# Kernel tuning notes

Measured on AMD Instinct MI355X. Metric: run time of the kernel, lower is better.

The kernel has to match this reference:

```python
import jax, jax.numpy as jnp
import numpy as np

C = 256  # channels
SHAPES = [(8, C, 80, 80), (8, C, 40, 40), (8, C, 20, 20), (8, C, 10, 10)]
EPS = 1e-8  # torch cosine_similarity eps


def _nearest_resize(x, H, W):
    # Matches F.interpolate(mode='nearest'): src_idx = floor(dst_idx * in/out)
    b, c, h, w = x.shape
    rows = (jnp.arange(H) * h) // H
    cols = (jnp.arange(W) * w) // W
    return x[:, :, rows[:, None], cols[None, :]]


def setup_inputs() -> dict:
    key = jax.random.key(0)
    ks = jax.random.split(key, 12)
    d = {}
    for i, s in enumerate(SHAPES):
        d[f"f{i}"] = jax.random.normal(ks[i], s, dtype=jnp.float32)
        d[f"w{i}"] = jax.random.normal(ks[4 + i], (C, C), dtype=jnp.float32) / jnp.sqrt(jnp.float32(C))
        d[f"b{i}"] = jax.random.normal(ks[8 + i], (C,), dtype=jnp.float32) * 0.01
    return d


def reference(f0, f1, f2, f3, w0, w1, w2, w3, b0, b1, b2, b3):
    feats = [f0, f1, f2, f3]
    ws = [w0, w1, w2, w3]
    bs = [b0, b1, b2, b3]
    H = max(f.shape[2] for f in feats)
    W = max(f.shape[3] for f in feats)
    proj = []
    for f, w, b in zip(feats, ws, bs):
        # 1x1 conv == per-pixel GEMM over channels
        p = jnp.einsum('bchw,oc->bohw', f, w) + b[None, :, None, None]
        if p.shape[2] != H or p.shape[3] != W:
            p = _nearest_resize(p, H, W)
        proj.append(p)
    B = proj[0].shape[0]
    N = len(proj)
    x = jnp.stack(proj, axis=1).reshape(B, N, C, H * W)  # [B,N,C,L]
    # Pairwise cosine similarity along channel dim at each spatial location,
    # then mean over locations (vectorized form of the O(N^2) torch loop).
    dot = jnp.einsum('bicl,bjcl->bijl', x, x)            # [B,N,N,L]
    nrm = jnp.sqrt(jnp.einsum('bicl,bicl->bil', x, x))   # [B,N,L]
    denom = jnp.maximum(nrm[:, :, None, :] * nrm[:, None, :, :], EPS)
    attn = (dot / denom).mean(axis=-1)                   # [B,N,N]
    return jax.nn.softmax(attn, axis=-1)
```

## Files before the change

kernel.cpp:

```cpp
#include <hip/hip_runtime.h>


#define CCH 256

typedef __attribute__((ext_vector_type(8))) short short8;
typedef __attribute__((ext_vector_type(4))) short short4_;
typedef __attribute__((ext_vector_type(4))) float float4_;

__device__ inline short f2bf(float x) {
    union { float f; unsigned u; } c; c.f = x;
    unsigned u = c.u + 0x7FFFu + ((c.u >> 16) & 1u);
    return (short)(u >> 16);
}
__device__ inline float bf2f(short b) {
    union { unsigned u; float f; } c; c.u = ((unsigned)(unsigned short)b) << 16;
    return c.f;
}

__global__ void pack_w(const float* __restrict__ w0, const float* __restrict__ w1,
                       const float* __restrict__ w2, const float* __restrict__ w3,
                       short* __restrict__ wp) {
    const float* W[4] = {w0, w1, w2, w3};
    const float* Ws = W[blockIdx.y];
    short* out = wp + (size_t)blockIdx.y * 65536;
    int base = (blockIdx.x * 256 + threadIdx.x) * 8;
    int kk0 = base & 31;
    int o   = (base >> 5) & 255;
    int ks  = base >> 13;
    const float* src = Ws + o * CCH + ks * 32 + kk0;
    short8 v;
#pragma unroll
    for (int j = 0; j < 8; ++j) v[j] = f2bf(src[j]);
    *(short8*)(out + base) = v;
}

#define LDP 56
#define TPITCH 264
__global__ __launch_bounds__(256) void proj_norm(
    const float* __restrict__ f0, const float* __restrict__ f1,
    const float* __restrict__ f2, const float* __restrict__ f3,
    const short* __restrict__ wp,
    const float* __restrict__ b0, const float* __restrict__ b1,
    const float* __restrict__ b2, const float* __restrict__ b3,
    short* __restrict__ u0, short* __restrict__ u1,
    short* __restrict__ u2, short* __restrict__ u3)
{
    __shared__ __align__(16) char smem[36864];
    short* Wt = (short*)smem;
    short* Ft = (short*)(smem + 28672);
    short* Ut = (short*)smem;

    const int blk = blockIdx.x;
    int s, b, tile, L;
    const float* F; const float* bias; short* U;
    if (blk < 800)       { s = 0; int r = blk;        b = r / 100; tile = r % 100; L = 6400; F = f0; bias = b0; U = u0; }
    else if (blk < 1000) { s = 1; int r = blk - 800;  b = r / 25;  tile = r % 25;  L = 1600; F = f1; bias = b1; U = u1; }
    else if (blk < 1056) { s = 2; int r = blk - 1000; b = r / 7;   tile = r % 7;   L = 400;  F = f2; bias = b2; U = u2; }
    else                 { s = 3; int r = blk - 1056; b = r / 2;   tile = r % 2;   L = 100;  F = f3; bias = b3; U = u3; }

    const int t    = threadIdx.x;
    const int lane = t & 63;
    const int wav  = t >> 6;
    const int ln   = lane & 15;
    const int quad = lane >> 4;
    const int pixbase = tile * 64;
    const float* Fb = F + (size_t)b * CCH * L;
    const short* wbase = wp + (size_t)s * 65536;

    float4_ acc[16];
#pragma unroll
    for (int i = 0; i < 16; ++i) acc[i] = (float4_){0.f, 0.f, 0.f, 0.f};

    const int fpix = t & 63;
    const int fk0  = (t >> 6) * 8;
    const int gpix0 = pixbase + fpix;
    const bool pin = gpix0 < L;

    for (int ks = 0; ks < 8; ++ks) {
        __syncthreads();
        {
            const short8* src = (const short8*)(wbase + ks * 8192);
#pragma unroll
            for (int it = 0; it < 4; ++it) {
                int idx = it * 256 + t;
                short8 v = src[idx];
                *(short8*)(&Wt[(idx >> 2) * LDP + (idx & 3) * 8]) = v;
            }
        }
        {
            const float* fs = Fb + (size_t)(ks * 32 + fk0) * L + gpix0;
            short8 v;
#pragma unroll
            for (int j = 0; j < 8; ++j)
                v[j] = f2bf(pin ? fs[(size_t)j * L] : 0.f);
            *(short8*)(&Ft[fpix * LDP + fk0]) = v;
        }
        __syncthreads();
        short8 bfrag = *(const short8*)(&Ft[(wav * 16 + ln) * LDP + quad * 8]);
#pragma unroll
        for (int mt = 0; mt < 16; ++mt) {
            short8 afrag = *(const short8*)(&Wt[(mt * 16 + ln) * LDP + quad * 8]);
            acc[mt] = __builtin_amdgcn_mfma_f32_16x16x32_bf16(afrag, bfrag, acc[mt], 0, 0, 0);
        }
    }

    float ss = 0.f;
#pragma unroll
    for (int mt = 0; mt < 16; ++mt) {
        float4_ bv = *(const float4_*)(bias + mt * 16 + quad * 4);
#pragma unroll
        for (int r = 0; r < 4; ++r) {
            float v = acc[mt][r] + bv[r];
            acc[mt][r] = v;
            ss += v * v;
        }
    }
    ss += __shfl_xor(ss, 16);
    ss += __shfl_xor(ss, 32);
    const float inv = 1.f / sqrtf(fmaxf(ss, 1e-24f));

    __syncthreads();

    const int pxl = wav * 16 + ln;
#pragma unroll
    for (int mt = 0; mt < 16; ++mt) {
        short4_ v;
#pragma unroll
        for (int r = 0; r < 4; ++r) v[r] = f2bf(acc[mt][r] * inv);
        *(short4_*)(&Ut[pxl * TPITCH + mt * 16 + quad * 4]) = v;
    }
    __syncthreads();

    {
        const int opx = t >> 2;
        const int c0 = (t & 3) * 64;
        const int gpx = pixbase + opx;
        if (gpx < L) {
            short* dst = U + ((size_t)b * L + gpx) * CCH + c0;
#pragma unroll
            for (int k = 0; k < 8; ++k)
                *(short8*)(dst + k * 8) = *(const short8*)(&Ut[opx * TPITCH + c0 + k * 8]);
        }
    }
}

template <int I>
__device__ inline void pair_body(const short* __restrict__ ui,
                                 const short* __restrict__ uu1,
                                 const short* __restrict__ uu2,
                                 const short* __restrict__ uu3,
                                 int b, int wave_id, int pg, int sub, float* acc) {
    constexpr int RI = 80 >> I;
    constexpr int LI = RI * RI;
    constexpr int NG = LI / 8;
    const short* __restrict__ uj[3] = {uu1, uu2, uu3};

    for (int g = wave_id; g < NG; g += 200) {
        const int px = g * 8 + pg;
        const int h = px / RI;
        const int w = px - h * RI;
        const short* pa = ui + ((size_t)(b * LI + px)) * CCH + sub * 32;
        float a[32];
#pragma unroll
        for (int k = 0; k < 4; ++k) {
            short8 v = *(const short8*)(pa + k * 8);
#pragma unroll
            for (int e = 0; e < 8; ++e) a[k * 8 + e] = bf2f(v[e]);
        }
#pragma unroll
        for (int d = 1; d <= 3 - I; ++d) {
            const int RJ = RI >> d;
            const int LJ = RJ * RJ;
            const int pxj = (h >> d) * RJ + (w >> d);
            const short* pb = uj[d - 1] + ((size_t)(b * LJ + pxj)) * CCH + sub * 32;
            float s = 0.f;
#pragma unroll
            for (int k = 0; k < 4; ++k) {
                short8 v = *(const short8*)(pb + k * 8);
#pragma unroll
                for (int e = 0; e < 8; ++e) s += a[k * 8 + e] * bf2f(v[e]);
            }
            acc[d - 1] += s;
        }
    }
}

__global__ __launch_bounds__(256) void pair_dots(
    const short* __restrict__ u0, const short* __restrict__ u1,
    const short* __restrict__ u2, const short* __restrict__ u3,
    float* __restrict__ sums) {
    const int i = blockIdx.y;
    const int b = blockIdx.z;
    const int t = threadIdx.x;
    const int lane = t & 63;
    const int wav = t >> 6;
    const int wave_id = blockIdx.x * 4 + wav;
    const int pg = lane >> 3;
    const int sub = lane & 7;

    float acc[3] = {0.f, 0.f, 0.f};
    if (i == 0)      pair_body<0>(u0, u1, u2, u3, b, wave_id, pg, sub, acc);
    else if (i == 1) pair_body<1>(u1, u2, u3, u3, b, wave_id, pg, sub, acc);
    else             pair_body<2>(u2, u3, u3, u3, b, wave_id, pg, sub, acc);

    __shared__ float red[4][3];
#pragma unroll
    for (int p = 0; p < 3; ++p) {
        float v = acc[p];
        v += __shfl_xor(v, 1);  v += __shfl_xor(v, 2);  v += __shfl_xor(v, 4);
        v += __shfl_xor(v, 8);  v += __shfl_xor(v, 16); v += __shfl_xor(v, 32);
        if (lane == 0) red[wav][p] = v;
    }
    __syncthreads();
    const int npairs = 3 - i;
    const int base = (i == 0) ? 0 : (i == 1) ? 3 : 5;
    if (t < npairs) {
        float s = red[0][t] + red[1][t] + red[2][t] + red[3][t];
        atomicAdd(&sums[b * 6 + base + t], s);
    }
}

__global__ void softmax4(const float* __restrict__ sums, float* __restrict__ out) {
    int t = threadIdx.x;
    if (t >= 128) return;
    int b = t >> 4, i = (t >> 2) & 3, j = t & 3;
    float a[4];
#pragma unroll
    for (int jj = 0; jj < 4; ++jj) {
        if (jj == i) { a[jj] = 1.0f; continue; }
        int lo = i < jj ? i : jj;
        int hi = i < jj ? jj : i;
        int pidx;
        if (lo == 0) pidx = hi - 1;
        else if (lo == 1) pidx = 1 + hi;
        else pidx = 5;
        int rf = 80 >> lo;
        a[jj] = sums[b * 6 + pidx] / (float)(rf * rf);
    }
    float m = fmaxf(fmaxf(a[0], a[1]), fmaxf(a[2], a[3]));
    float e0 = expf(a[0] - m), e1 = expf(a[1] - m), e2 = expf(a[2] - m), e3 = expf(a[3] - m);
    float sum = e0 + e1 + e2 + e3;
    float ev = (j == 0) ? e0 : (j == 1) ? e1 : (j == 2) ? e2 : e3;
    out[t] = ev / sum;
}

extern "C" void kernel_launch(void* const* d_in, const int* in_sizes, int n_in,
                              void* d_out, int out_size, void* d_ws, size_t ws_size,
                              hipStream_t stream) {
    const float* f[4]  = {(const float*)d_in[0], (const float*)d_in[3],
                          (const float*)d_in[6], (const float*)d_in[9]};
    const float* w[4]  = {(const float*)d_in[1], (const float*)d_in[4],
                          (const float*)d_in[7], (const float*)d_in[10]};
    const float* bs[4] = {(const float*)d_in[2], (const float*)d_in[5],
                          (const float*)d_in[8], (const float*)d_in[11]};

    const int Ls[4] = {6400, 1600, 400, 100};
    char* ws = (char*)d_ws;
    size_t off = 0;
    short* u[4];
    for (int s = 0; s < 4; ++s) {
        u[s] = (short*)(ws + off);
        off += (size_t)8 * CCH * Ls[s] * sizeof(short);
    }
    short* wp = (short*)(ws + off); off += 4 * 65536 * sizeof(short);
    float* sums = (float*)(ws + off);

    hipMemsetAsync(sums, 0, 64 * sizeof(float), stream);

    pack_w<<<dim3(32, 4), 256, 0, stream>>>(w[0], w[1], w[2], w[3], wp);

    proj_norm<<<1072, 256, 0, stream>>>(f[0], f[1], f[2], f[3], wp,
                                        bs[0], bs[1], bs[2], bs[3],
                                        u[0], u[1], u[2], u[3]);

    pair_dots<<<dim3(50, 3, 8), 256, 0, stream>>>(u[0], u[1], u[2], u[3], sums);

    softmax4<<<1, 128, 0, stream>>>(sums, (float*)d_out);
}
```

Before: 175.8 us.

## Pre-swizzle weights into MFMA fragment order and fuse pair dots per coarse cell

The packed weights and the staged feature tile are now stored in MFMA fragment order, so the LDS fills and fragment reads are contiguous and the shared-memory footprint shrinks, which should allow more resident blocks. The output transpose is done in two halves to fit the smaller LDS buffer. The pairwise dot kernel is reorganised around each coarsest-level cell, so every block loads the matching u1, u2 and u3 vectors once and reuses them across all fine pixels, computing all six pair sums in one pass instead of re-reading the coarse levels for each pair. The trade-offs are an extra barrier round in the epilogue and lower parallelism in the dot kernel (800 blocks).

```diff
diff --git a/kernel.cpp b/kernel.cpp
--- a/kernel.cpp
+++ b/kernel.cpp
@@ -23,18 +23,19 @@
     const float* W[4] = {w0, w1, w2, w3};
     const float* Ws = W[blockIdx.y];
     short* out = wp + (size_t)blockIdx.y * 65536;
-    int base = (blockIdx.x * 256 + threadIdx.x) * 8;
-    int kk0 = base & 31;
-    int o   = (base >> 5) & 255;
-    int ks  = base >> 13;
-    const float* src = Ws + o * CCH + ks * 32 + kk0;
+    int id = blockIdx.x * 256 + threadIdx.x;
+    int ks = id >> 10;
+    int rest = id & 1023;
+    int mt = rest >> 6;
+    int fl = rest & 63;
+    int ln = fl & 15, quad = fl >> 4;
+    const float* src = Ws + (mt * 16 + ln) * CCH + ks * 32 + quad * 8;
     short8 v;
 #pragma unroll
     for (int j = 0; j < 8; ++j) v[j] = f2bf(src[j]);
-    *(short8*)(out + base) = v;
-}
-
-#define LDP 56
+    *(short8*)(out + (size_t)id * 8) = v;
+}
+
 #define TPITCH 264
 __global__ __launch_bounds__(256) void proj_norm(
     const float* __restrict__ f0, const float* __restrict__ f1,
@@ -45,9 +46,9 @@
     short* __restrict__ u0, short* __restrict__ u1,
     short* __restrict__ u2, short* __restrict__ u3)
 {
-    __shared__ __align__(16) char smem[36864];
+    __shared__ __align__(16) char smem[20992];
     short* Wt = (short*)smem;
-    short* Ft = (short*)(smem + 28672);
+    short* Ft = (short*)(smem + 16384);
     short* Ut = (short*)smem;
 
     const int blk = blockIdx.x;
@@ -72,34 +73,36 @@
     for (int i = 0; i < 16; ++i) acc[i] = (float4_){0.f, 0.f, 0.f, 0.f};
 
     const int fpix = t & 63;
-    const int fk0  = (t >> 6) * 8;
+    const int fchunk = t >> 6;
     const int gpix0 = pixbase + fpix;
     const bool pin = gpix0 < L;
+    const int gl0 = pin ? gpix0 : 0;
+    short* fdst = Ft + (fpix >> 4) * 512 + (fchunk * 16 + (fpix & 15)) * 8;
 
     for (int ks = 0; ks < 8; ++ks) {
         __syncthreads();
         {
             const short8* src = (const short8*)(wbase + ks * 8192);
+            short8* dst = (short8*)Wt;
 #pragma unroll
             for (int it = 0; it < 4; ++it) {
                 int idx = it * 256 + t;
-                short8 v = src[idx];
-                *(short8*)(&Wt[(idx >> 2) * LDP + (idx & 3) * 8]) = v;
+                dst[idx] = src[idx];
             }
         }
         {
-            const float* fs = Fb + (size_t)(ks * 32 + fk0) * L + gpix0;
+            const float* fs = Fb + (size_t)(ks * 32 + fchunk * 8) * L + gl0;
             short8 v;
 #pragma unroll
             for (int j = 0; j < 8; ++j)
-                v[j] = f2bf(pin ? fs[(size_t)j * L] : 0.f);
-            *(short8*)(&Ft[fpix * LDP + fk0]) = v;
-        }
-        __syncthreads();
-        short8 bfrag = *(const short8*)(&Ft[(wav * 16 + ln) * LDP + quad * 8]);
+                v[j] = pin ? f2bf(fs[(size_t)j * L]) : (short)0;
+            *(short8*)fdst = v;
+        }
+        __syncthreads();
+        short8 bfrag = *(const short8*)(Ft + wav * 512 + lane * 8);
 #pragma unroll
         for (int mt = 0; mt < 16; ++mt) {
-            short8 afrag = *(const short8*)(&Wt[(mt * 16 + ln) * LDP + quad * 8]);
+            short8 afrag = *(const short8*)(Wt + mt * 512 + lane * 8);
             acc[mt] = __builtin_amdgcn_mfma_f32_16x16x32_bf16(afrag, bfrag, acc[mt], 0, 0, 0);
         }
     }
@@ -119,105 +122,113 @@
     ss += __shfl_xor(ss, 32);
     const float inv = 1.f / sqrtf(fmaxf(ss, 1e-24f));
 
-    __syncthreads();
-
     const int pxl = wav * 16 + ln;
 #pragma unroll
-    for (int mt = 0; mt < 16; ++mt) {
-        short4_ v;
-#pragma unroll
-        for (int r = 0; r < 4; ++r) v[r] = f2bf(acc[mt][r] * inv);
-        *(short4_*)(&Ut[pxl * TPITCH + mt * 16 + quad * 4]) = v;
-    }
-    __syncthreads();
-
-    {
-        const int opx = t >> 2;
-        const int c0 = (t & 3) * 64;
-        const int gpx = pixbase + opx;
+    for (int p = 0; p < 2; ++p) {
+        __syncthreads();
+        if ((pxl >> 5) == p) {
+#pragma unroll
+            for (int mt = 0; mt < 16; ++mt) {
+                short4_ v;
+#pragma unroll
+                for (int r = 0; r < 4; ++r) v[r] = f2bf(acc[mt][r] * inv);
+                *(short4_*)(&Ut[(pxl & 31) * TPITCH + mt * 16 + quad * 4]) = v;
+            }
+        }
+        __syncthreads();
+        const int opx = t >> 3;
+        const int c0 = (t & 7) * 32;
+        const int gpx = pixbase + p * 32 + opx;
         if (gpx < L) {
             short* dst = U + ((size_t)b * L + gpx) * CCH + c0;
 #pragma unroll
-            for (int k = 0; k < 8; ++k)
+            for (int k = 0; k < 4; ++k)
                 *(short8*)(dst + k * 8) = *(const short8*)(&Ut[opx * TPITCH + c0 + k * 8]);
         }
     }
 }
 
-template <int I>
-__device__ inline void pair_body(const short* __restrict__ ui,
-                                 const short* __restrict__ uu1,
-                                 const short* __restrict__ uu2,
-                                 const short* __restrict__ uu3,
-                                 int b, int wave_id, int pg, int sub, float* acc) {
-    constexpr int RI = 80 >> I;
-    constexpr int LI = RI * RI;
-    constexpr int NG = LI / 8;
-    const short* __restrict__ uj[3] = {uu1, uu2, uu3};
-
-    for (int g = wave_id; g < NG; g += 200) {
-        const int px = g * 8 + pg;
-        const int h = px / RI;
-        const int w = px - h * RI;
-        const short* pa = ui + ((size_t)(b * LI + px)) * CCH + sub * 32;
-        float a[32];
-#pragma unroll
-        for (int k = 0; k < 4; ++k) {
-            short8 v = *(const short8*)(pa + k * 8);
-#pragma unroll
-            for (int e = 0; e < 8; ++e) a[k * 8 + e] = bf2f(v[e]);
-        }
-#pragma unroll
-        for (int d = 1; d <= 3 - I; ++d) {
-            const int RJ = RI >> d;
-            const int LJ = RJ * RJ;
-            const int pxj = (h >> d) * RJ + (w >> d);
-            const short* pb = uj[d - 1] + ((size_t)(b * LJ + pxj)) * CCH + sub * 32;
-            float s = 0.f;
-#pragma unroll
-            for (int k = 0; k < 4; ++k) {
-                short8 v = *(const short8*)(pb + k * 8);
-#pragma unroll
-                for (int e = 0; e < 8; ++e) s += a[k * 8 + e] * bf2f(v[e]);
-            }
-            acc[d - 1] += s;
-        }
-    }
-}
-
-__global__ __launch_bounds__(256) void pair_dots(
+__global__ __launch_bounds__(256) void cell_dots(
     const short* __restrict__ u0, const short* __restrict__ u1,
     const short* __restrict__ u2, const short* __restrict__ u3,
     float* __restrict__ sums) {
-    const int i = blockIdx.y;
-    const int b = blockIdx.z;
-    const int t = threadIdx.x;
-    const int lane = t & 63;
-    const int wav = t >> 6;
-    const int wave_id = blockIdx.x * 4 + wav;
-    const int pg = lane >> 3;
-    const int sub = lane & 7;
-
-    float acc[3] = {0.f, 0.f, 0.f};
-    if (i == 0)      pair_body<0>(u0, u1, u2, u3, b, wave_id, pg, sub, acc);
-    else if (i == 1) pair_body<1>(u1, u2, u3, u3, b, wave_id, pg, sub, acc);
-    else             pair_body<2>(u2, u3, u3, u3, b, wave_id, pg, sub, acc);
-
-    __shared__ float red[4][3];
-#pragma unroll
-    for (int p = 0; p < 3; ++p) {
-        float v = acc[p];
+    const int b  = blockIdx.y;
+    const int c3 = blockIdx.x;
+    const int H3 = c3 / 10, W3 = c3 - H3 * 10;
+    const int t  = threadIdx.x;
+    const int c1 = t >> 4;
+    const int k  = t & 15;
+    const int h1 = c1 >> 2, w1 = c1 & 3;
+    const int r1 = 4 * H3 + h1, q1 = 4 * W3 + w1;
+    const int px1 = r1 * 40 + q1;
+    const int px2 = (2 * H3 + (h1 >> 1)) * 20 + (2 * W3 + (w1 >> 1));
+    const int px3 = H3 * 10 + W3;
+
+    float b1v[16], b2v[16], b3v[16];
+    {
+        const short* p1 = u1 + ((size_t)(b * 1600 + px1)) * CCH + k * 16;
+        const short* p2 = u2 + ((size_t)(b * 400  + px2)) * CCH + k * 16;
+        const short* p3 = u3 + ((size_t)(b * 100  + px3)) * CCH + k * 16;
+#pragma unroll
+        for (int h = 0; h < 2; ++h) {
+            short8 v1 = *(const short8*)(p1 + h * 8);
+            short8 v2 = *(const short8*)(p2 + h * 8);
+            short8 v3 = *(const short8*)(p3 + h * 8);
+#pragma unroll
+            for (int e = 0; e < 8; ++e) {
+                b1v[h * 8 + e] = bf2f(v1[e]);
+                b2v[h * 8 + e] = bf2f(v2[e]);
+                b3v[h * 8 + e] = bf2f(v3[e]);
+            }
+        }
+    }
+
+    float d01 = 0.f, d02 = 0.f, d03 = 0.f;
+#pragma unroll
+    for (int dh = 0; dh < 2; ++dh) {
+#pragma unroll
+        for (int dw = 0; dw < 2; ++dw) {
+            const int px0 = (2 * r1 + dh) * 80 + 2 * q1 + dw;
+            const short* pa = u0 + ((size_t)(b * 6400 + px0)) * CCH + k * 16;
+            float av[16];
+#pragma unroll
+            for (int h = 0; h < 2; ++h) {
+                short8 v = *(const short8*)(pa + h * 8);
+#pragma unroll
+                for (int e = 0; e < 8; ++e) av[h * 8 + e] = bf2f(v[e]);
+            }
+#pragma unroll
+            for (int e = 0; e < 16; ++e) {
+                d01 += av[e] * b1v[e];
+                d02 += av[e] * b2v[e];
+                d03 += av[e] * b3v[e];
+            }
+        }
+    }
+    float d12 = 0.f, d13 = 0.f, d23 = 0.f;
+#pragma unroll
+    for (int e = 0; e < 16; ++e) {
+        d12 += b1v[e] * b2v[e];
+        d13 += b1v[e] * b3v[e];
+    }
+    if (((h1 & 1) | (w1 & 1)) == 0) {
+#pragma unroll
+        for (int e = 0; e < 16; ++e) d23 += b2v[e] * b3v[e];
+    }
+
+    float vals[6] = {d01, d02, d03, d12, d13, d23};
+    __shared__ float red[4][6];
+    const int lane = t & 63, wav = t >> 6;
+#pragma unroll
+    for (int p = 0; p < 6; ++p) {
+        float v = vals[p];
         v += __shfl_xor(v, 1);  v += __shfl_xor(v, 2);  v += __shfl_xor(v, 4);
         v += __shfl_xor(v, 8);  v += __shfl_xor(v, 16); v += __shfl_xor(v, 32);
         if (lane == 0) red[wav][p] = v;
     }
     __syncthreads();
-    const int npairs = 3 - i;
-    const int base = (i == 0) ? 0 : (i == 1) ? 3 : 5;
-    if (t < npairs) {
-        float s = red[0][t] + red[1][t] + red[2][t] + red[3][t];
-        atomicAdd(&sums[b * 6 + base + t], s);
-    }
+    if (t < 6)
+        atomicAdd(&sums[b * 6 + t], red[0][t] + red[1][t] + red[2][t] + red[3][t]);
 }
 
 __global__ void softmax4(const float* __restrict__ sums, float* __restrict__ out) {
@@ -273,7 +284,7 @@
                                         bs[0], bs[1], bs[2], bs[3],
                                         u[0], u[1], u[2], u[3]);
 
-    pair_dots<<<dim3(50, 3, 8), 256, 0, stream>>>(u[0], u[1], u[2], u[3], sums);
+    cell_dots<<<dim3(100, 8), 256, 0, stream>>>(u[0], u[1], u[2], u[3], sums);
 
     softmax4<<<1, 128, 0, stream>>>(sums, (float*)d_out);
 }
```

New measurement: 243.5 us. 1.39x slower.
